# Optimization experiments

Measured on AMD Instinct MI355X. Metric: run time of the kernel, lower is better.

## Reference

```python
import jax, jax.numpy as jnp
import numpy as np

DIM = 384
HEADS = 6
HEAD_DIM = 64
WIN = 14
SCALE = HEAD_DIM ** -0.5
EPS = 1e-5  # torch LayerNorm default


def setup_inputs() -> dict:
    key = jax.random.key(0)
    ks = jax.random.split(key, 8)
    w = lambda k, shape: jax.random.normal(k, shape, dtype=jnp.float32) * 0.02
    return {
        "x": jax.random.normal(ks[0], (1, 336, 336, DIM), dtype=jnp.float32),
        "qkv_w": w(ks[1], (DIM, 3 * DIM)),
        "qkv_b": jnp.zeros((3 * DIM,), jnp.float32),
        "proj_w": w(ks[2], (DIM, DIM)),
        "proj_b": jnp.zeros((DIM,), jnp.float32),
        "rel_pos_h": w(ks[3], (2 * WIN - 1, HEAD_DIM)),
        "rel_pos_w": w(ks[4], (2 * WIN - 1, HEAD_DIM)),
        "norm1_w": jnp.ones((DIM,), jnp.float32),
        "norm1_b": jnp.zeros((DIM,), jnp.float32),
        "norm2_w": jnp.ones((DIM,), jnp.float32),
        "norm2_b": jnp.zeros((DIM,), jnp.float32),
        "fc1_w": w(ks[5], (DIM, 4 * DIM)),
        "fc1_b": jnp.zeros((4 * DIM,), jnp.float32),
        "fc2_w": w(ks[6], (4 * DIM, DIM)),
        "fc2_b": jnp.zeros((DIM,), jnp.float32),
    }


def _layernorm(x, w, b):
    m = jnp.mean(x, axis=-1, keepdims=True)
    v = jnp.var(x, axis=-1, keepdims=True)
    return (x - m) / jnp.sqrt(v + EPS) * w + b


def _rel_table(rel_pos):
    coords = np.arange(WIN)[:, None] - np.arange(WIN)[None, :] + (WIN - 1)
    return rel_pos[coords]


def _block(x, qkv_w, qkv_b, proj_w, proj_b, rel_pos_h, rel_pos_w,
           norm1_w, norm1_b, norm2_w, norm2_b, fc1_w, fc1_b, fc2_w, fc2_b):
    B, H, W, C = x.shape
    shortcut = x
    x = _layernorm(x, norm1_w, norm1_b)

    nH, nW = H // WIN, W // WIN
    xw = x.reshape(B, nH, WIN, nW, WIN, C).transpose(0, 1, 3, 2, 4, 5)
    xw = xw.reshape(B * nH * nW, WIN * WIN, C)  # [Nw, 196, C]
    Nw, L = xw.shape[0], WIN * WIN

    # --- attention with decomposed rel-pos ---
    qkv = xw @ qkv_w + qkv_b                         # [Nw, 196, 3C]
    qkv = qkv.reshape(Nw, L, 3, HEADS, HEAD_DIM).transpose(2, 0, 3, 1, 4)
    q, k, v = qkv[0], qkv[1], qkv[2]                 # [Nw, h, 196, d]

    attn = jnp.einsum("bhqd,bhkd->bhqk", q * SCALE, k)  # [Nw, h, 196, 196]

    Rh = _rel_table(rel_pos_h)                       # [14, 14, d]
    Rw = _rel_table(rel_pos_w)
    r_q = q.reshape(Nw, HEADS, WIN, WIN, HEAD_DIM)
    rel_h = jnp.einsum("bnhwc,hkc->bnhwk", r_q, Rh)  # [Nw, h, 14, 14, 14]
    rel_w = jnp.einsum("bnhwc,wkc->bnhwk", r_q, Rw)
    attn = (attn.reshape(Nw, HEADS, WIN, WIN, WIN, WIN)
            + rel_h[..., :, None] + rel_w[..., None, :]).reshape(Nw, HEADS, L, L)

    attn = jax.nn.softmax(attn, axis=-1)
    out = jnp.einsum("bhqk,bhkd->bhqd", attn, v)     # [Nw, h, 196, d]
    out = out.transpose(0, 2, 1, 3).reshape(Nw, L, C)
    out = out @ proj_w + proj_b

    # --- window unpartition ---
    out = out.reshape(B, nH, nW, WIN, WIN, C).transpose(0, 1, 3, 2, 4, 5)
    out = out.reshape(B, H, W, C)

    x = shortcut + out
    h = _layernorm(x, norm2_w, norm2_b)
    h = jax.nn.gelu(h @ fc1_w + fc1_b, approximate=False) @ fc2_w + fc2_b
    return x + h


def reference(x, qkv_w, qkv_b, proj_w, proj_b, rel_pos_h, rel_pos_w,
              norm1_w, norm1_b, norm2_w, norm2_b, fc1_w, fc1_b, fc2_w, fc2_b):
    return _block(x, qkv_w, qkv_b, proj_w, proj_b, rel_pos_h, rel_pos_w,
                  norm1_w, norm1_b, norm2_w, norm2_b, fc1_w, fc1_b, fc2_w, fc2_b)
```

## Files before the change

### kernel.cpp

```cpp
#include <hip/hip_runtime.h>
#include <math.h>

#define TOKENS 112896
#define C      384
#define NQKV   1152
#define NFC    1536
#define HEADS  6
#define HD     64
#define WIN    14
#define L      196
#define NWS    24
#define SCALEF 0.125f

typedef unsigned int  u32;
typedef unsigned short u16;
typedef short short8 __attribute__((ext_vector_type(8)));
typedef float floatx4 __attribute__((ext_vector_type(4)));

__device__ __forceinline__ u16 f2bf(float f) {
  u32 u = __float_as_uint(f);
  u += 0x7FFFu + ((u >> 16) & 1u);
  return (u16)(u >> 16);
}

__device__ __forceinline__ float bf2f(u16 v) {
  return __uint_as_float((u32)v << 16);
}

__device__ __forceinline__ void async16(u16* lds, const u16* g) {
  __builtin_amdgcn_global_load_lds((const __attribute__((address_space(1))) void*)g,
                                   (__attribute__((address_space(3))) void*)lds,
                                   16, 0, 0);
}

__device__ __forceinline__ int win_to_tok(int r) {
  int n = r / L, l = r % L;
  int wh = n / NWS, ww = n % NWS;
  int ih = l / WIN, iw = l % WIN;
  return (wh * WIN + ih) * 336 + ww * WIN + iw;
}

__global__ __launch_bounds__(256) void conv_t_kernel(const float* __restrict__ in,
    u16* __restrict__ out, int K, int N)
{
  __shared__ u16 tile[32][33];
  const int kb = blockIdx.y * 32, nb = blockIdx.x * 32;
  const int tx = threadIdx.x & 31, ty = threadIdx.x >> 5;
#pragma unroll
  for (int i = 0; i < 4; i++) {
    int k = kb + ty + i * 8;
    tile[ty + i * 8][tx] = f2bf(in[(size_t)k * N + nb + tx]);
  }
  __syncthreads();
#pragma unroll
  for (int i = 0; i < 4; i++) {
    int n = nb + ty + i * 8;
    out[(size_t)n * K + kb + tx] = tile[tx][ty + i * 8];
  }
}

template<bool PERMUTE>
__global__ __launch_bounds__(128) void ln_kernel(const float* __restrict__ x,
    const float* __restrict__ w, const float* __restrict__ b,
    u16* __restrict__ out)
{
  const int t = blockIdx.x;
  const int tid = threadIdx.x;
  const float* xr = x + (size_t)t * C;
  float v0 = xr[tid], v1 = xr[tid + 128], v2 = xr[tid + 256];
  float s  = v0 + v1 + v2;
  float ss = v0 * v0 + v1 * v1 + v2 * v2;
#pragma unroll
  for (int off = 32; off > 0; off >>= 1) {
    s  += __shfl_down(s, off);
    ss += __shfl_down(ss, off);
  }
  __shared__ float red[4];
  if ((tid & 63) == 0) { red[(tid >> 6) * 2 + 0] = s; red[(tid >> 6) * 2 + 1] = ss; }
  __syncthreads();
  float S  = red[0] + red[2];
  float SS = red[1] + red[3];
  float mean = S * (1.0f / C);
  float var  = SS * (1.0f / C) - mean * mean;
  float rstd = rsqrtf(var + 1e-5f);
  size_t orow;
  if (PERMUTE) {
    int h_ = t / 336, w_ = t % 336;
    int wh = h_ / WIN, ih = h_ % WIN;
    int ww = w_ / WIN, iw = w_ % WIN;
    orow = (size_t)((wh * NWS + ww) * L + ih * WIN + iw);
  } else {
    orow = (size_t)t;
  }
  u16* op = out + orow * C;
  op[tid]       = f2bf((v0 - mean) * rstd * w[tid]       + b[tid]);
  op[tid + 128] = f2bf((v1 - mean) * rstd * w[tid + 128] + b[tid + 128]);
  op[tid + 256] = f2bf((v2 - mean) * rstd * w[tid + 256] + b[tid + 256]);
}

template<int MODE>
__global__ __launch_bounds__(256, 2) void gemm_bf16(
    const u16* __restrict__ A, const u16* __restrict__ Bt,
    const float* __restrict__ bias, const float* __restrict__ res,
    void* __restrict__ outv, int N, int K)
{
  __shared__ u16 As[2][128 * 64];
  __shared__ u16 Bs[2][128 * 64];
  const int tid = threadIdx.x;
  const int w = tid >> 6, l = tid & 63;

  const int nwg = gridDim.x * gridDim.y;
  int lin = blockIdx.y * gridDim.x + blockIdx.x;
  {
    int q8 = nwg >> 3, r8 = nwg & 7;
    int xcd = lin & 7, sub = lin >> 3;
    lin = (xcd < r8 ? xcd * (q8 + 1) : r8 * (q8 + 1) + (xcd - r8) * q8) + sub;
  }
  const int bx = lin % gridDim.x, by = lin / gridDim.x;
  const int bm = by * 128, bn = bx * 128;

  const int wm = (w >> 1) * 64, wn = (w & 1) * 64;
  const int lm = l & 15, quad = l >> 4;

  floatx4 acc[4][4] = {};

  const int srow8 = l >> 3;
  const int sgran = (l & 7) ^ srow8;
  const u16* Ag[4];
  const u16* Bg[4];
#pragma unroll
  for (int p = 0; p < 4; p++) {
    Ag[p] = A  + (size_t)(bm + p * 32 + w * 8 + srow8) * K + sgran * 8;
    Bg[p] = Bt + (size_t)(bn + p * 32 + w * 8 + srow8) * K + sgran * 8;
  }

  auto stage = [&](int buf, int kt) {
#pragma unroll
    for (int p = 0; p < 4; p++) {
      async16(&As[buf][(p * 32 + w * 8) * 64], Ag[p] + kt);
      async16(&Bs[buf][(p * 32 + w * 8) * 64], Bg[p] + kt);
    }
  };

  const int nk = K >> 6;
  stage(0, 0);
  __syncthreads();

  for (int t = 0; t < nk; t++) {
    const int buf = t & 1;
    if (t + 1 < nk) stage(buf ^ 1, (t + 1) << 6);

    short8 af[4][2], bf[4][2];
#pragma unroll
    for (int i = 0; i < 4; i++) {
      int r = wm + i * 16 + lm, sw = r & 7;
      af[i][0] = *(const short8*)(&As[buf][r * 64 + ((quad ^ sw) * 8)]);
      af[i][1] = *(const short8*)(&As[buf][r * 64 + (((4 + quad) ^ sw) * 8)]);
    }
#pragma unroll
    for (int j = 0; j < 4; j++) {
      int r = wn + j * 16 + lm, sw = r & 7;
      bf[j][0] = *(const short8*)(&Bs[buf][r * 64 + ((quad ^ sw) * 8)]);
      bf[j][1] = *(const short8*)(&Bs[buf][r * 64 + (((4 + quad) ^ sw) * 8)]);
    }
#pragma unroll
    for (int i = 0; i < 4; i++)
#pragma unroll
      for (int j = 0; j < 4; j++) {
        acc[i][j] = __builtin_amdgcn_mfma_f32_16x16x32_bf16(af[i][0], bf[j][0], acc[i][j], 0, 0, 0);
        acc[i][j] = __builtin_amdgcn_mfma_f32_16x16x32_bf16(af[i][1], bf[j][1], acc[i][j], 0, 0, 0);
      }
    __syncthreads();
  }

  const int colbase = bn + wn + lm;
  float bb[4];
#pragma unroll
  for (int j = 0; j < 4; j++) bb[j] = bias[colbase + j * 16];

#pragma unroll
  for (int i = 0; i < 4; i++) {
#pragma unroll
    for (int reg = 0; reg < 4; reg++) {
      int row = bm + wm + i * 16 + quad * 4 + reg;
      size_t ro;
      if (MODE == 1) ro = (size_t)win_to_tok(row) * N;
      else           ro = (size_t)row * N;
#pragma unroll
      for (int j = 0; j < 4; j++) {
        float v = acc[i][j][reg] + bb[j];
        int col = colbase + j * 16;
        if (MODE == 0) {
          ((u16*)outv)[ro + col] = f2bf(v);
        } else if (MODE == 1) {
          ((float*)outv)[ro + col] = v + res[ro + col];
        } else if (MODE == 2) {
          ((u16*)outv)[ro + col] = f2bf(0.5f * v * (1.0f + erff(v * 0.70710678118654752f)));
        } else {
          ((float*)outv)[ro + col] = v + res[ro + col];
        }
      }
    }
  }
}

__global__ __launch_bounds__(256, 2) void attn_kernel(
    const u16* __restrict__ qkv,
    const float* __restrict__ relh, const float* __restrict__ relw,
    u16* __restrict__ out)
{
  __shared__ float Plds[4][512];
  __shared__ u16 rhlds[208 * 28];
  __shared__ u16 rwlds[208 * 28];
  __shared__ u16 Klds[32 * 64];
  __shared__ u16 Vtl[64 * 40];

  const int n = blockIdx.x / HEADS;
  const int h = blockIdx.x % HEADS;
  const int tid = threadIdx.x;
  const int w = tid >> 6;
  const int l = tid & 63;
  const int lm = l & 15;
  const int quad = l >> 4;
  const size_t base = (size_t)n * L;

  short8 qf[4][2];
#pragma unroll
  for (int i = 0; i < 4; i++) {
    int rt = w + 4 * i;
    if (rt <= 12) {
      int row = rt * 16 + lm; if (row > 195) row = 195;
      const u16* qp = qkv + (base + row) * NQKV + h * HD + quad * 8;
#pragma unroll
      for (int kf = 0; kf < 2; kf++)
        qf[i][kf] = *(const short8*)(qp + kf * 32);
    }
  }

  {
    short8 tf[2][2][2];
#pragma unroll
    for (int tab = 0; tab < 2; tab++) {
      const float* tp = tab ? relw : relh;
#pragma unroll
      for (int ct = 0; ct < 2; ct++) {
        int t = ct * 16 + lm;
#pragma unroll
        for (int kf = 0; kf < 2; kf++) {
          short8 v = {0, 0, 0, 0, 0, 0, 0, 0};
          if (t < 27) {
            const float* p = tp + t * HD + kf * 32 + quad * 8;
            float4 a = *(const float4*)p;
            float4 b = *(const float4*)(p + 4);
            v[0] = (short)f2bf(a.x); v[1] = (short)f2bf(a.y);
            v[2] = (short)f2bf(a.z); v[3] = (short)f2bf(a.w);
            v[4] = (short)f2bf(b.x); v[5] = (short)f2bf(b.y);
            v[6] = (short)f2bf(b.z); v[7] = (short)f2bf(b.w);
          }
          tf[tab][ct][kf] = v;
        }
      }
    }
#pragma unroll
    for (int i = 0; i < 4; i++) {
      int rt = w + 4 * i;
      if (rt > 12) continue;
#pragma unroll
      for (int tab = 0; tab < 2; tab++) {
        u16* dst = tab ? rwlds : rhlds;
#pragma unroll
        for (int ct = 0; ct < 2; ct++) {
          floatx4 acc = {};
          acc = __builtin_amdgcn_mfma_f32_16x16x32_bf16(qf[i][0], tf[tab][ct][0], acc, 0, 0, 0);
          acc = __builtin_amdgcn_mfma_f32_16x16x32_bf16(qf[i][1], tf[tab][ct][1], acc, 0, 0, 0);
          int t = ct * 16 + lm;
          if (t < 28) {
#pragma unroll
            for (int reg = 0; reg < 4; reg++) {
              int q = rt * 16 + quad * 4 + reg;
              dst[q * 28 + t] = f2bf(acc[reg]);
            }
          }
        }
      }
    }
  }

  floatx4 oacc[4][4] = {};
  float lsum[4][4] = {};

#pragma unroll 1
  for (int ks = 0; ks < 7; ks++) {
    __syncthreads();
    {
      int r = tid >> 3, g = tid & 7;
      int row = ks * 32 + r; if (row > 195) row = 195;
      uint4 kd = *(const uint4*)(qkv + (base + row) * NQKV + C + h * HD + g * 8);
      *(uint4*)&Klds[r * 64 + ((g ^ (r & 7)) * 8)] = kd;
    }
    {
      int r = tid & 31, seg = tid >> 5;
      int row = ks * 32 + r; if (row > 195) row = 195;
      uint4 vd = *(const uint4*)(qkv + (base + row) * NQKV + 2 * C + h * HD + seg * 8);
      union { uint4 u; u16 s[8]; } vv; vv.u = vd;
#pragma unroll
      for (int j = 0; j < 8; j++) Vtl[(seg * 8 + j) * 40 + r] = vv.s[j];
    }
    __syncthreads();

    short8 kfr[2][2];
#pragma unroll
    for (int ct = 0; ct < 2; ct++) {
      int krow = ct * 16 + lm;
#pragma unroll
      for (int kf = 0; kf < 2; kf++)
        kfr[ct][kf] = *(const short8*)&Klds[krow * 64 + (((kf * 4 + quad) ^ (krow & 7)) * 8)];
    }
    short8 vfr[4];
#pragma unroll
    for (int dt = 0; dt < 4; dt++)
      vfr[dt] = *(const short8*)&Vtl[(dt * 16 + lm) * 40 + quad * 8];

#pragma unroll
    for (int i = 0; i < 4; i++) {
      int rt = w + 4 * i;
      if (rt > 12) continue;
      floatx4 sc[2] = {};
#pragma unroll
      for (int ct = 0; ct < 2; ct++) {
        sc[ct] = __builtin_amdgcn_mfma_f32_16x16x32_bf16(qf[i][0], kfr[ct][0], sc[ct], 0, 0, 0);
        sc[ct] = __builtin_amdgcn_mfma_f32_16x16x32_bf16(qf[i][1], kfr[ct][1], sc[ct], 0, 0, 0);
      }
      float* Pw = Plds[w];
#pragma unroll
      for (int ct = 0; ct < 2; ct++) {
        int k = ks * 32 + ct * 16 + lm;
        int kh = (k * 293) >> 12;
        int kw2 = k - kh * 14;
        bool kval = (k < 196);
#pragma unroll
        for (int reg = 0; reg < 4; reg++) {
          int q = rt * 16 + quad * 4 + reg;
          int qh = (q * 293) >> 12;
          int qw = q - qh * 14;
          int th = qh - kh + 13; th = th < 0 ? 0 : th;
          int tw = qw - kw2 + 13;
          float bh = bf2f(rhlds[q * 28 + th]);
          float bw = bf2f(rwlds[q * 28 + tw]);
          float s = sc[ct][reg] * SCALEF + bh + bw;
          float p = kval ? __expf(s) : 0.0f;
          lsum[i][reg] += p;
          int prow = quad * 4 + reg;
          int col = ct * 16 + lm;
          Pw[prow * 32 + (((col >> 2) ^ (prow & 7)) * 4) + (col & 3)] = p;
        }
      }
      floatx4 pa = *(const floatx4*)&Pw[lm * 32 + (((2 * quad) ^ (lm & 7)) * 4)];
      floatx4 pb = *(const floatx4*)&Pw[lm * 32 + (((2 * quad + 1) ^ (lm & 7)) * 4)];
      short8 pfr;
#pragma unroll
      for (int j = 0; j < 4; j++) {
        pfr[j]     = (short)f2bf(pa[j]);
        pfr[4 + j] = (short)f2bf(pb[j]);
      }
#pragma unroll
      for (int dt = 0; dt < 4; dt++)
        oacc[i][dt] = __builtin_amdgcn_mfma_f32_16x16x32_bf16(pfr, vfr[dt], oacc[i][dt], 0, 0, 0);
    }
  }

#pragma unroll
  for (int i = 0; i < 4; i++) {
    int rt = w + 4 * i;
    if (rt > 12) continue;
#pragma unroll
    for (int reg = 0; reg < 4; reg++) {
      float v = lsum[i][reg];
      v += __shfl_xor(v, 1);
      v += __shfl_xor(v, 2);
      v += __shfl_xor(v, 4);
      v += __shfl_xor(v, 8);
      float inv = 1.0f / v;
      int row = rt * 16 + quad * 4 + reg;
      if (row < 196) {
        u16* op = out + (base + row) * C + h * HD + lm;
#pragma unroll
        for (int dt = 0; dt < 4; dt++) op[dt * 16] = f2bf(oacc[i][dt][reg] * inv);
      }
    }
  }
}

extern "C" void kernel_launch(void* const* d_in, const int* in_sizes, int n_in,
                              void* d_out, int out_size, void* d_ws, size_t ws_size,
                              hipStream_t stream)
{
  const float* x      = (const float*)d_in[0];
  const float* qkv_w  = (const float*)d_in[1];
  const float* qkv_b  = (const float*)d_in[2];
  const float* proj_w = (const float*)d_in[3];
  const float* proj_b = (const float*)d_in[4];
  const float* rel_h  = (const float*)d_in[5];
  const float* rel_w  = (const float*)d_in[6];
  const float* n1w    = (const float*)d_in[7];
  const float* n1b    = (const float*)d_in[8];
  const float* n2w    = (const float*)d_in[9];
  const float* n2b    = (const float*)d_in[10];
  const float* fc1_w  = (const float*)d_in[11];
  const float* fc1_b  = (const float*)d_in[12];
  const float* fc2_w  = (const float*)d_in[13];
  const float* fc2_b  = (const float*)d_in[14];

  u16*  W0 = (u16*)d_ws;
  u16*  W1 = (u16*)((char*)d_ws + 86704128);
  float* W2 = (float*)((char*)d_ws + 86704128 + 346816512);
  u16*  WT = (u16*)((char*)d_ws + 86704128 + 346816512 + 173408256);
  u16* qkv_wT  = WT;
  u16* proj_wT = qkv_wT + 442368;
  u16* fc1_wT  = proj_wT + 147456;
  u16* fc2_wT  = fc1_wT + 589824;

  conv_t_kernel<<<dim3(NQKV / 32, C / 32), 256, 0, stream>>>(qkv_w, qkv_wT, C, NQKV);
  conv_t_kernel<<<dim3(C / 32, C / 32), 256, 0, stream>>>(proj_w, proj_wT, C, C);
  conv_t_kernel<<<dim3(NFC / 32, C / 32), 256, 0, stream>>>(fc1_w, fc1_wT, C, NFC);
  conv_t_kernel<<<dim3(C / 32, NFC / 32), 256, 0, stream>>>(fc2_w, fc2_wT, NFC, C);

  ln_kernel<true><<<TOKENS, 128, 0, stream>>>(x, n1w, n1b, W0);
  gemm_bf16<0><<<dim3(NQKV / 128, TOKENS / 128), 256, 0, stream>>>(
      W0, qkv_wT, qkv_b, nullptr, W1, NQKV, C);
  attn_kernel<<<576 * HEADS, 256, 0, stream>>>(W1, rel_h, rel_w, W0);
  gemm_bf16<1><<<dim3(C / 128, TOKENS / 128), 256, 0, stream>>>(
      W0, proj_wT, proj_b, x, W2, C, C);
  ln_kernel<false><<<TOKENS, 128, 0, stream>>>(W2, n2w, n2b, W0);
  gemm_bf16<2><<<dim3(NFC / 128, TOKENS / 128), 256, 0, stream>>>(
      W0, fc1_wT, fc1_b, nullptr, W1, NFC, C);
  gemm_bf16<3><<<dim3(C / 128, TOKENS / 128), 256, 0, stream>>>(
      W1, fc2_wT, fc2_b, W2, (float*)d_out, C, NFC);
}
```

Baseline: 1.482 ms.

## Halve GEMM K-tile to raise occupancy and use fast polynomial GELU

Result: faster. 1.386 ms (-6.5%).

```diff
diff --git a/kernel.cpp b/kernel.cpp
--- a/kernel.cpp
+++ b/kernel.cpp
@@ -25,6 +25,16 @@
 
 __device__ __forceinline__ float bf2f(u16 v) {
   return __uint_as_float((u32)v << 16);
+}
+
+__device__ __forceinline__ float gelu_f(float v) {
+  float z = fabsf(v) * 0.70710678118654752f;
+  float t = 1.0f / (1.0f + 0.3275911f * z);
+  float poly = t * (0.254829592f + t * (-0.284496736f + t * (1.421413741f +
+               t * (-1.453152027f + t * 1.061405429f))));
+  float erfv = 1.0f - poly * __expf(-z * z);
+  erfv = copysignf(erfv, v);
+  return 0.5f * v * (1.0f + erfv);
 }
 
 __device__ __forceinline__ void async16(u16* lds, const u16* g) {
@@ -99,13 +109,13 @@
 }
 
 template<int MODE>
-__global__ __launch_bounds__(256, 2) void gemm_bf16(
+__global__ __launch_bounds__(256, 4) void gemm_bf16(
     const u16* __restrict__ A, const u16* __restrict__ Bt,
     const float* __restrict__ bias, const float* __restrict__ res,
     void* __restrict__ outv, int N, int K)
 {
-  __shared__ u16 As[2][128 * 64];
-  __shared__ u16 Bs[2][128 * 64];
+  __shared__ u16 As[2][128 * 32];
+  __shared__ u16 Bs[2][128 * 32];
   const int tid = threadIdx.x;
   const int w = tid >> 6, l = tid & 63;
 
@@ -124,52 +134,57 @@
 
   floatx4 acc[4][4] = {};
 
-  const int srow8 = l >> 3;
-  const int sgran = (l & 7) ^ srow8;
-  const u16* Ag[4];
-  const u16* Bg[4];
-#pragma unroll
-  for (int p = 0; p < 4; p++) {
-    Ag[p] = A  + (size_t)(bm + p * 32 + w * 8 + srow8) * K + sgran * 8;
-    Bg[p] = Bt + (size_t)(bn + p * 32 + w * 8 + srow8) * K + sgran * 8;
-  }
+  const u16* Asrc[2]; const u16* Bsrc[2];
+#pragma unroll
+  for (int q = 0; q < 2; q++) {
+    int t = q * 256 + tid;
+    int r = t >> 2, gl = t & 3;
+    int sg = gl ^ ((r >> 1) & 3);
+    Asrc[q] = A  + (size_t)(bm + r) * K + sg * 8;
+    Bsrc[q] = Bt + (size_t)(bn + r) * K + sg * 8;
+  }
+  u16* Ad[2]; u16* Bd[2];
+#pragma unroll
+  for (int q = 0; q < 2; q++) {
+    Ad[q] = &As[0][(q * 256 + w * 64) * 8];
+    Bd[q] = &Bs[0][(q * 256 + w * 64) * 8];
+  }
+  const int bufoff = 128 * 32;
 
   auto stage = [&](int buf, int kt) {
 #pragma unroll
-    for (int p = 0; p < 4; p++) {
-      async16(&As[buf][(p * 32 + w * 8) * 64], Ag[p] + kt);
-      async16(&Bs[buf][(p * 32 + w * 8) * 64], Bg[p] + kt);
+    for (int q = 0; q < 2; q++) {
+      async16(Ad[q] + buf * bufoff, Asrc[q] + kt);
+      async16(Bd[q] + buf * bufoff, Bsrc[q] + kt);
     }
   };
 
-  const int nk = K >> 6;
+  const int xg = (quad ^ ((lm >> 1) & 3)) * 8;
+  const u16* ard[4]; const u16* brd[4];
+#pragma unroll
+  for (int i = 0; i < 4; i++) {
+    ard[i] = &As[0][(wm + i * 16 + lm) * 32 + xg];
+    brd[i] = &Bs[0][(wn + i * 16 + lm) * 32 + xg];
+  }
+
+  const int nk = K >> 5;
   stage(0, 0);
   __syncthreads();
 
   for (int t = 0; t < nk; t++) {
     const int buf = t & 1;
-    if (t + 1 < nk) stage(buf ^ 1, (t + 1) << 6);
-
-    short8 af[4][2], bf[4][2];
+    if (t + 1 < nk) stage(buf ^ 1, (t + 1) << 5);
+    const int bo = buf * bufoff;
+    short8 bfr[4];
+#pragma unroll
+    for (int j = 0; j < 4; j++) bfr[j] = *(const short8*)(brd[j] + bo);
 #pragma unroll
     for (int i = 0; i < 4; i++) {
-      int r = wm + i * 16 + lm, sw = r & 7;
-      af[i][0] = *(const short8*)(&As[buf][r * 64 + ((quad ^ sw) * 8)]);
-      af[i][1] = *(const short8*)(&As[buf][r * 64 + (((4 + quad) ^ sw) * 8)]);
-    }
-#pragma unroll
-    for (int j = 0; j < 4; j++) {
-      int r = wn + j * 16 + lm, sw = r & 7;
-      bf[j][0] = *(const short8*)(&Bs[buf][r * 64 + ((quad ^ sw) * 8)]);
-      bf[j][1] = *(const short8*)(&Bs[buf][r * 64 + (((4 + quad) ^ sw) * 8)]);
-    }
-#pragma unroll
-    for (int i = 0; i < 4; i++)
-#pragma unroll
-      for (int j = 0; j < 4; j++) {
-        acc[i][j] = __builtin_amdgcn_mfma_f32_16x16x32_bf16(af[i][0], bf[j][0], acc[i][j], 0, 0, 0);
-        acc[i][j] = __builtin_amdgcn_mfma_f32_16x16x32_bf16(af[i][1], bf[j][1], acc[i][j], 0, 0, 0);
-      }
+      short8 afr = *(const short8*)(ard[i] + bo);
+#pragma unroll
+      for (int j = 0; j < 4; j++)
+        acc[i][j] = __builtin_amdgcn_mfma_f32_16x16x32_bf16(afr, bfr[j], acc[i][j], 0, 0, 0);
+    }
     __syncthreads();
   }
 
@@ -195,7 +210,7 @@
         } else if (MODE == 1) {
           ((float*)outv)[ro + col] = v + res[ro + col];
         } else if (MODE == 2) {
-          ((u16*)outv)[ro + col] = f2bf(0.5f * v * (1.0f + erff(v * 0.70710678118654752f)));
+          ((u16*)outv)[ro + col] = f2bf(gelu_f(v));
         } else {
           ((float*)outv)[ro + col] = v + res[ro + col];
         }
```
